# Performance work log

Hardware: AMD Instinct MI355X
Metric: run time of the kernel (lower is better)

The kernel has to match this reference:

```python
import jax, jax.numpy as jnp
import numpy as np

B, D_INNER, D_STATE, DT_RANK = 1024, 2560, 16, 160


def setup_inputs() -> dict:
    key = jax.random.key(0)
    ks = jax.random.split(key, 9)
    s = lambda n: 1.0 / np.sqrt(n)
    return {
        "x": jax.random.normal(ks[0], (B, D_INNER), jnp.float32),
        "h": jax.random.normal(ks[1], (B, D_INNER, D_STATE), jnp.float32),
        "W_dt_low": jax.random.normal(ks[2], (DT_RANK, D_INNER), jnp.float32) * s(D_INNER),
        "W_dt": jax.random.normal(ks[3], (D_INNER, DT_RANK), jnp.float32) * s(DT_RANK),
        "b_dt": jax.random.normal(ks[4], (D_INNER,), jnp.float32),
        "W_B": jax.random.normal(ks[5], (D_STATE, D_INNER), jnp.float32) * s(D_INNER),
        "W_C": jax.random.normal(ks[6], (D_STATE, D_INNER), jnp.float32) * s(D_INNER),
        "A_log": jax.random.uniform(ks[7], (D_INNER, D_STATE), jnp.float32, 0.0, 1.0),
        "D": jax.random.normal(ks[8], (D_INNER,), jnp.float32),
    }


def reference(x, h, W_dt_low, W_dt, b_dt, W_B, W_C, A_log, D):
    # Single-token Mamba selective-scan step (decode).
    # dt projections: d_inner -> dt_rank -> d_inner, then softplus
    dt = jax.nn.softplus(jnp.einsum('bd,rd->br', x, W_dt_low) @ W_dt.T + b_dt)  # [B, D_INNER]
    Bt = jnp.einsum('bd,nd->bn', x, W_B)  # [B, D_STATE]
    Ct = jnp.einsum('bd,nd->bn', x, W_C)  # [B, D_STATE]
    A = -jnp.exp(A_log)                   # [D_INNER, D_STATE]
    delta_A = jnp.exp(dt[:, :, None] * A[None])                 # [B, D_INNER, D_STATE]
    delta_B_x = dt[:, :, None] * Bt[:, None, :] * x[:, :, None] # [B, D_INNER, D_STATE]
    h_new = delta_A * h + delta_B_x
    y = jnp.einsum('bdn,bn->bd', h_new, Ct) + D * x             # [B, D_INNER]
    return y
```

## Files before the change

### kernel.cpp

```cpp
#include <hip/hip_runtime.h>
#include <hip/hip_bf16.h>
#include <math.h>

#define B_SZ    1024
#define DI      2560
#define DS      16
#define DR      160
#define NPROJ   192

typedef __bf16 bf16x8 __attribute__((ext_vector_type(8)));
typedef float  f32x4  __attribute__((ext_vector_type(4)));

__device__ __forceinline__ float fast_exp2(float x) {
#if __has_builtin(__builtin_amdgcn_exp2f)
  return __builtin_amdgcn_exp2f(x);
#else
  return exp2f(x);
#endif
}
__device__ __forceinline__ float fast_log2(float x) {
#if __has_builtin(__builtin_amdgcn_logf)
  return __builtin_amdgcn_logf(x);
#else
  return log2f(x);
#endif
}

#define LOG2E 1.44269504088896f
#define LN2   0.693147180559945f

__global__ void __launch_bounds__(256) convert_kernel(
    const float* __restrict__ x, const float* __restrict__ Wdl,
    const float* __restrict__ WB, const float* __restrict__ WC,
    const float* __restrict__ Wdt, const float* __restrict__ A_log,
    __bf16* __restrict__ xb, __bf16* __restrict__ wcat,
    __bf16* __restrict__ wdtb, float* __restrict__ negA2) {
  int i = blockIdx.x * 256 + threadIdx.x;
  const int NX   = B_SZ * DI;
  const int NWDL = DR * DI;
  const int NWB  = DS * DI;
  const int NWDT = DI * DR;
  const int NA   = DI * DS;
  if (i < NX)   { xb[i] = (__bf16)x[i]; return; }
  i -= NX;
  if (i < NWDL) { wcat[i] = (__bf16)Wdl[i]; return; }
  i -= NWDL;
  if (i < NWB)  { wcat[NWDL + i] = (__bf16)WB[i]; return; }
  i -= NWB;
  if (i < NWB)  { wcat[NWDL + NWB + i] = (__bf16)WC[i]; return; }
  i -= NWB;
  if (i < NWDT) { wdtb[i] = (__bf16)Wdt[i]; return; }
  i -= NWDT;
  if (i < NA)   { negA2[i] = -fast_exp2(A_log[i] * LOG2E) * LOG2E; }
}

__global__ void __launch_bounds__(64) proj_kernel(
    const __bf16* __restrict__ xb, const __bf16* __restrict__ wcat,
    __bf16* __restrict__ dtlow, float* __restrict__ Bt, float* __restrict__ Ct) {
  int gw    = blockIdx.x;
  int lane  = threadIdx.x;
  int mtile = gw & 63;
  int ntile = gw >> 6;
  int b0 = mtile * 16, n0 = ntile * 16;
  int m = lane & 15, quad = lane >> 4;
  const __bf16* ap = xb   + (size_t)(b0 + m) * DI + quad * 8;
  const __bf16* bp = wcat + (size_t)(n0 + m) * DI + quad * 8;
  f32x4 acc = {0.f, 0.f, 0.f, 0.f};
#pragma unroll 4
  for (int k0 = 0; k0 < DI; k0 += 32) {
    bf16x8 a = *(const bf16x8*)(ap + k0);
    bf16x8 b = *(const bf16x8*)(bp + k0);
    acc = __builtin_amdgcn_mfma_f32_16x16x32_bf16(a, b, acc, 0, 0, 0);
  }
  int nn = n0 + m;
#pragma unroll
  for (int r = 0; r < 4; ++r) {
    int bb = b0 + quad * 4 + r;
    float v = acc[r];
    if (nn < DR)            dtlow[bb * DR + nn] = (__bf16)v;
    else if (nn < DR + DS)  Bt[bb * DS + (nn - DR)] = v;
    else                    Ct[bb * DS + (nn - DR - DS)] = v;
  }
}

__global__ void __launch_bounds__(256) dtssm_kernel(
    const __bf16* __restrict__ dtlow, const __bf16* __restrict__ wdtb,
    const float* __restrict__ b_dt, const float* __restrict__ x,
    const float* __restrict__ h, const float* __restrict__ negA2,
    const float* __restrict__ Bt, const float* __restrict__ Ct,
    const float* __restrict__ Dp, float* __restrict__ y) {
  int gw    = blockIdx.x * 4 + (threadIdx.x >> 6);
  int lane  = threadIdx.x & 63;
  int mtile = gw & 63;
  int ntile = gw >> 6;
  int b0 = mtile * 16, d0 = ntile * 16;
  int m = lane & 15, quad = lane >> 4;

  const __bf16* ap = dtlow + (size_t)(b0 + m) * DR + quad * 8;
  const __bf16* bp = wdtb  + (size_t)(d0 + m) * DR + quad * 8;
  f32x4 acc = {0.f, 0.f, 0.f, 0.f};
#pragma unroll
  for (int k0 = 0; k0 < DR; k0 += 32) {
    bf16x8 a = *(const bf16x8*)(ap + k0);
    bf16x8 b = *(const bf16x8*)(bp + k0);
    acc = __builtin_amdgcn_mfma_f32_16x16x32_bf16(a, b, acc, 0, 0, 0);
  }

  int dd = d0 + m;
  float bias = b_dt[dd];
  float dv   = Dp[dd];
  const float4* a4 = (const float4*)(negA2 + (size_t)dd * DS);
  float4 av0 = a4[0], av1 = a4[1], av2 = a4[2], av3 = a4[3];

#pragma unroll
  for (int r = 0; r < 4; ++r) {
    int bb = b0 + quad * 4 + r;
    float z = acc[r] + bias;
    float t = fast_exp2(z * LOG2E);
    float dt = (z > 80.f) ? z : fast_log2(1.f + t) * LN2;

    size_t e = (size_t)bb * DI + dd;
    float xv  = x[e];
    float dxv = dt * xv;
    const float4* h4 = (const float4*)(h  + e * DS);
    const float4* b4 = (const float4*)(Bt + (size_t)bb * DS);
    const float4* c4 = (const float4*)(Ct + (size_t)bb * DS);
    float s = 0.f;
#pragma unroll
    for (int j = 0; j < 4; ++j) {
      float4 hv = h4[j], bv = b4[j], cv = c4[j];
      float4 avj = (j == 0) ? av0 : (j == 1) ? av1 : (j == 2) ? av2 : av3;
      s += (fast_exp2(avj.x * dt) * hv.x + bv.x * dxv) * cv.x;
      s += (fast_exp2(avj.y * dt) * hv.y + bv.y * dxv) * cv.y;
      s += (fast_exp2(avj.z * dt) * hv.z + bv.z * dxv) * cv.z;
      s += (fast_exp2(avj.w * dt) * hv.w + bv.w * dxv) * cv.w;
    }
    y[e] = s + dv * xv;
  }
}

extern "C" void kernel_launch(void* const* d_in, const int* in_sizes, int n_in,
                              void* d_out, int out_size, void* d_ws, size_t ws_size,
                              hipStream_t stream) {
  const float* x     = (const float*)d_in[0];
  const float* h     = (const float*)d_in[1];
  const float* Wdl   = (const float*)d_in[2];
  const float* Wdt   = (const float*)d_in[3];
  const float* b_dt  = (const float*)d_in[4];
  const float* WB    = (const float*)d_in[5];
  const float* WC    = (const float*)d_in[6];
  const float* A_log = (const float*)d_in[7];
  const float* Dp    = (const float*)d_in[8];
  float* y = (float*)d_out;

  char* ws = (char*)d_ws;
  __bf16* xb    = (__bf16*)(ws);
  __bf16* wcat  = (__bf16*)(ws + 5242880);
  __bf16* wdtb  = (__bf16*)(ws + 6225920);
  float*  negA2 = (float*) (ws + 7045120);
  __bf16* dtlow = (__bf16*)(ws + 7208960);
  float*  Bt    = (float*) (ws + 7536640);
  float*  Ct    = (float*) (ws + 7602176);
  if (ws_size < 7667712) return;

  convert_kernel<<<13920, 256, 0, stream>>>(x, Wdl, WB, WC, Wdt, A_log,
                                            xb, wcat, wdtb, negA2);
  proj_kernel<<<768, 64, 0, stream>>>(xb, wcat, dtlow, Bt, Ct);
  dtssm_kernel<<<2560, 256, 0, stream>>>(dtlow, wdtb, b_dt, x, h, negA2,
                                         Bt, Ct, Dp, y);
}
```

Baseline: 295.9 us.

## Fold bf16 conversion kernel into projection and scan kernels

Removes the separate conversion kernel and instead converts fp32 x and weights to bf16 on the fly inside the MFMA loops. The -exp(A_log) precomputation moves into the scan kernel. This drops one launch and a full write-then-read round trip of bf16 copies. In exchange, fp32 operands are loaded at twice the bytes inside the GEMM loops, and the A_log exp is recomputed per tile.

```diff
diff --git a/kernel.cpp b/kernel.cpp
--- a/kernel.cpp
+++ b/kernel.cpp
@@ -6,7 +6,6 @@
 #define DI      2560
 #define DS      16
 #define DR      160
-#define NPROJ   192
 
 typedef __bf16 bf16x8 __attribute__((ext_vector_type(8)));
 typedef float  f32x4  __attribute__((ext_vector_type(4)));
@@ -29,33 +28,18 @@
 #define LOG2E 1.44269504088896f
 #define LN2   0.693147180559945f
 
-__global__ void __launch_bounds__(256) convert_kernel(
-    const float* __restrict__ x, const float* __restrict__ Wdl,
-    const float* __restrict__ WB, const float* __restrict__ WC,
-    const float* __restrict__ Wdt, const float* __restrict__ A_log,
-    __bf16* __restrict__ xb, __bf16* __restrict__ wcat,
-    __bf16* __restrict__ wdtb, float* __restrict__ negA2) {
-  int i = blockIdx.x * 256 + threadIdx.x;
-  const int NX   = B_SZ * DI;
-  const int NWDL = DR * DI;
-  const int NWB  = DS * DI;
-  const int NWDT = DI * DR;
-  const int NA   = DI * DS;
-  if (i < NX)   { xb[i] = (__bf16)x[i]; return; }
-  i -= NX;
-  if (i < NWDL) { wcat[i] = (__bf16)Wdl[i]; return; }
-  i -= NWDL;
-  if (i < NWB)  { wcat[NWDL + i] = (__bf16)WB[i]; return; }
-  i -= NWB;
-  if (i < NWB)  { wcat[NWDL + NWB + i] = (__bf16)WC[i]; return; }
-  i -= NWB;
-  if (i < NWDT) { wdtb[i] = (__bf16)Wdt[i]; return; }
-  i -= NWDT;
-  if (i < NA)   { negA2[i] = -fast_exp2(A_log[i] * LOG2E) * LOG2E; }
+__device__ __forceinline__ bf16x8 cvt8(const float* __restrict__ p) {
+  float4 v0 = *(const float4*)p;
+  float4 v1 = *(const float4*)(p + 4);
+  bf16x8 r;
+  r[0] = (__bf16)v0.x; r[1] = (__bf16)v0.y; r[2] = (__bf16)v0.z; r[3] = (__bf16)v0.w;
+  r[4] = (__bf16)v1.x; r[5] = (__bf16)v1.y; r[6] = (__bf16)v1.z; r[7] = (__bf16)v1.w;
+  return r;
 }
 
 __global__ void __launch_bounds__(64) proj_kernel(
-    const __bf16* __restrict__ xb, const __bf16* __restrict__ wcat,
+    const float* __restrict__ x, const float* __restrict__ Wdl,
+    const float* __restrict__ WB, const float* __restrict__ WC,
     __bf16* __restrict__ dtlow, float* __restrict__ Bt, float* __restrict__ Ct) {
   int gw    = blockIdx.x;
   int lane  = threadIdx.x;
@@ -63,16 +47,21 @@
   int ntile = gw >> 6;
   int b0 = mtile * 16, n0 = ntile * 16;
   int m = lane & 15, quad = lane >> 4;
-  const __bf16* ap = xb   + (size_t)(b0 + m) * DI + quad * 8;
-  const __bf16* bp = wcat + (size_t)(n0 + m) * DI + quad * 8;
+  int nn = n0 + m;
+  const float* ap = x + (size_t)(b0 + m) * DI + quad * 8;
+  const float* wrow;
+  if (nn < DR)            wrow = Wdl + (size_t)nn * DI;
+  else if (nn < DR + DS)  wrow = WB  + (size_t)(nn - DR) * DI;
+  else                    wrow = WC  + (size_t)(nn - DR - DS) * DI;
+  const float* bp = wrow + quad * 8;
+
   f32x4 acc = {0.f, 0.f, 0.f, 0.f};
 #pragma unroll 4
   for (int k0 = 0; k0 < DI; k0 += 32) {
-    bf16x8 a = *(const bf16x8*)(ap + k0);
-    bf16x8 b = *(const bf16x8*)(bp + k0);
+    bf16x8 a = cvt8(ap + k0);
+    bf16x8 b = cvt8(bp + k0);
     acc = __builtin_amdgcn_mfma_f32_16x16x32_bf16(a, b, acc, 0, 0, 0);
   }
-  int nn = n0 + m;
 #pragma unroll
   for (int r = 0; r < 4; ++r) {
     int bb = b0 + quad * 4 + r;
@@ -84,9 +73,9 @@
 }
 
 __global__ void __launch_bounds__(256) dtssm_kernel(
-    const __bf16* __restrict__ dtlow, const __bf16* __restrict__ wdtb,
+    const __bf16* __restrict__ dtlow, const float* __restrict__ Wdt,
     const float* __restrict__ b_dt, const float* __restrict__ x,
-    const float* __restrict__ h, const float* __restrict__ negA2,
+    const float* __restrict__ h, const float* __restrict__ A_log,
     const float* __restrict__ Bt, const float* __restrict__ Ct,
     const float* __restrict__ Dp, float* __restrict__ y) {
   int gw    = blockIdx.x * 4 + (threadIdx.x >> 6);
@@ -95,22 +84,33 @@
   int ntile = gw >> 6;
   int b0 = mtile * 16, d0 = ntile * 16;
   int m = lane & 15, quad = lane >> 4;
+  int dd = d0 + m;
 
   const __bf16* ap = dtlow + (size_t)(b0 + m) * DR + quad * 8;
-  const __bf16* bp = wdtb  + (size_t)(d0 + m) * DR + quad * 8;
+  const float*  bp = Wdt   + (size_t)dd * DR + quad * 8;
   f32x4 acc = {0.f, 0.f, 0.f, 0.f};
 #pragma unroll
   for (int k0 = 0; k0 < DR; k0 += 32) {
     bf16x8 a = *(const bf16x8*)(ap + k0);
-    bf16x8 b = *(const bf16x8*)(bp + k0);
+    bf16x8 b = cvt8(bp + k0);
     acc = __builtin_amdgcn_mfma_f32_16x16x32_bf16(a, b, acc, 0, 0, 0);
   }
 
-  int dd = d0 + m;
   float bias = b_dt[dd];
   float dv   = Dp[dd];
-  const float4* a4 = (const float4*)(negA2 + (size_t)dd * DS);
-  float4 av0 = a4[0], av1 = a4[1], av2 = a4[2], av3 = a4[3];
+  const float4* al4 = (const float4*)(A_log + (size_t)dd * DS);
+  float4 av0, av1, av2, av3;
+  {
+    float4 l0 = al4[0], l1 = al4[1], l2 = al4[2], l3 = al4[3];
+    av0.x = -fast_exp2(l0.x * LOG2E) * LOG2E; av0.y = -fast_exp2(l0.y * LOG2E) * LOG2E;
+    av0.z = -fast_exp2(l0.z * LOG2E) * LOG2E; av0.w = -fast_exp2(l0.w * LOG2E) * LOG2E;
+    av1.x = -fast_exp2(l1.x * LOG2E) * LOG2E; av1.y = -fast_exp2(l1.y * LOG2E) * LOG2E;
+    av1.z = -fast_exp2(l1.z * LOG2E) * LOG2E; av1.w = -fast_exp2(l1.w * LOG2E) * LOG2E;
+    av2.x = -fast_exp2(l2.x * LOG2E) * LOG2E; av2.y = -fast_exp2(l2.y * LOG2E) * LOG2E;
+    av2.z = -fast_exp2(l2.z * LOG2E) * LOG2E; av2.w = -fast_exp2(l2.w * LOG2E) * LOG2E;
+    av3.x = -fast_exp2(l3.x * LOG2E) * LOG2E; av3.y = -fast_exp2(l3.y * LOG2E) * LOG2E;
+    av3.z = -fast_exp2(l3.z * LOG2E) * LOG2E; av3.w = -fast_exp2(l3.w * LOG2E) * LOG2E;
+  }
 
 #pragma unroll
   for (int r = 0; r < 4; ++r) {
@@ -154,18 +154,12 @@
   float* y = (float*)d_out;
 
   char* ws = (char*)d_ws;
-  __bf16* xb    = (__bf16*)(ws);
-  __bf16* wcat  = (__bf16*)(ws + 5242880);
-  __bf16* wdtb  = (__bf16*)(ws + 6225920);
-  float*  negA2 = (float*) (ws + 7045120);
-  __bf16* dtlow = (__bf16*)(ws + 7208960);
-  float*  Bt    = (float*) (ws + 7536640);
-  float*  Ct    = (float*) (ws + 7602176);
-  if (ws_size < 7667712) return;
+  __bf16* dtlow = (__bf16*)(ws);
+  float*  Bt    = (float*) (ws + 327680);
+  float*  Ct    = (float*) (ws + 393216);
+  if (ws_size < 458752) return;
 
-  convert_kernel<<<13920, 256, 0, stream>>>(x, Wdl, WB, WC, Wdt, A_log,
-                                            xb, wcat, wdtb, negA2);
-  proj_kernel<<<768, 64, 0, stream>>>(xb, wcat, dtlow, Bt, Ct);
-  dtssm_kernel<<<2560, 256, 0, stream>>>(dtlow, wdtb, b_dt, x, h, negA2,
+  proj_kernel<<<768, 64, 0, stream>>>(x, Wdl, WB, WC, dtlow, Bt, Ct);
+  dtssm_kernel<<<2560, 256, 0, stream>>>(dtlow, Wdt, b_dt, x, h, A_log,
                                          Bt, Ct, Dp, y);
 }
```

After: 349.6 us. 1.18x slower.
